# Optimization experiments

Hardware: AMD Instinct MI355X
Metric: run time of the kernel (lower is better)

The kernel has to match this reference:

```python
import jax, jax.numpy as jnp
import numpy as np

B, S, V, D = 8, 1024, 8192, 256
MAX_POS = 1024


def _positional_encoding(position, d_model):
    pos = np.arange(position)[:, None].astype(np.float32)
    i = np.arange(d_model)[None, :].astype(np.float32)
    angle_rads = pos / np.power(10000.0, 2.0 * np.floor(i / 2.0) / np.float32(d_model))
    angle_rads[:, 0::2] = np.sin(angle_rads[:, 0::2])
    angle_rads[:, 1::2] = np.cos(angle_rads[:, 1::2])
    return jnp.asarray(angle_rads[None, ...], dtype=jnp.float32)  # [1, position, d_model]


def setup_inputs() -> dict:
    key = jax.random.key(0)
    k1, k2 = jax.random.split(key)
    x = jax.random.randint(k1, (B, S, V), 0, 2, dtype=jnp.int32)  # multi-hot mask
    emb_table = jax.random.normal(k2, (V, D), dtype=jnp.float32) * 0.02
    pos_enc = _positional_encoding(MAX_POS, D)
    return {"x": x, "emb_table": emb_table, "pos_enc": pos_enc}


def reference(x, emb_table, pos_enc):
    # Multi-hot embedding-bag: sum_v x[b,s,v] * emb_table[v,:]  (dense O(V) reduction,
    # faithful to get_emb's full-vocab embed * mask + reduce_sum)
    seq_len = x.shape[1]
    d_model = emb_table.shape[1]
    xf = x.astype(jnp.float32)
    emb = jnp.einsum('bsv,vd->bsd', xf, emb_table)
    emb = emb * jnp.sqrt(jnp.float32(d_model))
    # positional encoding gated by whether the position has any active token
    any_tok = (jnp.sum(x, axis=-1) > 0).astype(jnp.float32)[..., None]  # [B,S,1]
    out = emb + pos_enc[:, :seq_len, :] * any_tok
    # dropout is identity in eval mode; num_layers = 0 -> no encoder layers
    return out
```

## Files before the change

kernel.cpp:

```cpp
#include <hip/hip_runtime.h>


#define M_TOT 8192
#define K_TOT 8192
#define D_DIM 256
#define KSPLIT 4
#define KCHUNK (K_TOT / KSPLIT)
#define BK 32

typedef short  short8  __attribute__((ext_vector_type(8)));
typedef float  floatx4 __attribute__((ext_vector_type(4)));
typedef int    intx4   __attribute__((ext_vector_type(4)));

#define WS_RS_OFF (4u * 1024u * 1024u)

__global__ __launch_bounds__(256) void zero_kernel(float* __restrict__ out, int* __restrict__ rs) {
    int b = blockIdx.x;
    if (b < 2048) {
        floatx4 z = {0.f, 0.f, 0.f, 0.f};
        *(floatx4*)(out + ((size_t)b * 256 + threadIdx.x) * 4) = z;
    } else {
        intx4 z = {0, 0, 0, 0};
        *(intx4*)(rs + ((size_t)(b - 2048) * 256 + threadIdx.x) * 4) = z;
    }
}

__global__ __launch_bounds__(256) void prep_kernel(const float* __restrict__ emb,
                                                   unsigned short* __restrict__ wsB) {
    __shared__ unsigned short tile[64][72];
    int v0 = blockIdx.x * 64, d0 = blockIdx.y * 64;
    int t = threadIdx.x;
    int r = t >> 2, c0 = (t & 3) * 16;
    const float* src = emb + (size_t)(v0 + r) * D_DIM + d0 + c0;
#pragma unroll
    for (int i = 0; i < 16; ++i) {
        unsigned int u = __float_as_uint(src[i] * 16.0f);
        u += 0x7fffu + ((u >> 16) & 1u);
        tile[c0 + i][r] = (unsigned short)(u >> 16);
    }
    __syncthreads();
    unsigned short* dst = wsB + (size_t)(d0 + r) * K_TOT + v0 + c0;
#pragma unroll
    for (int i = 0; i < 16; ++i) dst[i] = tile[r][c0 + i];
}

__global__ __launch_bounds__(256) void gemm_kernel(const int* __restrict__ x,
                                                   const unsigned short* __restrict__ wsB,
                                                   float* __restrict__ out,
                                                   int* __restrict__ rs) {
    __shared__ unsigned short Al[64][40];

    const int m0   = blockIdx.x * 64;
    const int kbeg = blockIdx.y * KCHUNK;
    const int t    = threadIdx.x;
    const int wave = t >> 6, lane = t & 63;
    const int quad = lane >> 4, rl = lane & 15;
    const int n0   = wave * 64;

    const int arow = t >> 2, akp = (t & 3) * 8;
    const int* aptr = x + (size_t)(m0 + arow) * K_TOT + kbeg + akp;

    floatx4 acc[4][4];
#pragma unroll
    for (int i = 0; i < 4; ++i)
#pragma unroll
        for (int j = 0; j < 4; ++j) acc[i][j] = (floatx4){0.f, 0.f, 0.f, 0.f};

    int rsum = 0;

    for (int kk = 0; kk < KCHUNK; kk += BK) {
        intx4 a0 = *(const intx4*)aptr;
        intx4 a1 = *(const intx4*)(aptr + 4);
        aptr += BK;

        short8 bf[4];
#pragma unroll
        for (int j = 0; j < 4; ++j) {
            const unsigned short* bp = wsB + (size_t)(n0 + j * 16 + rl) * K_TOT + kbeg + kk + quad * 8;
            bf[j] = *(const short8*)bp;
        }

        short8 av;
#pragma unroll
        for (int i = 0; i < 4; ++i) { av[i]     = a0[i] ? (short)0x3F80 : (short)0; rsum += a0[i]; }
#pragma unroll
        for (int i = 0; i < 4; ++i) { av[4 + i] = a1[i] ? (short)0x3F80 : (short)0; rsum += a1[i]; }

        __syncthreads();
        *(short8*)&Al[arow][akp] = av;
        __syncthreads();

        short8 af[4];
#pragma unroll
        for (int i = 0; i < 4; ++i)
            af[i] = *(const short8*)&Al[i * 16 + rl][quad * 8];

#pragma unroll
        for (int i = 0; i < 4; ++i)
#pragma unroll
            for (int j = 0; j < 4; ++j)
                acc[i][j] = __builtin_amdgcn_mfma_f32_16x16x32_bf16(af[i], bf[j], acc[i][j], 0, 0, 0);
    }

    rsum += __shfl_down(rsum, 1);
    rsum += __shfl_down(rsum, 2);
    if ((t & 3) == 0) atomicAdd(&rs[m0 + arow], rsum);

#pragma unroll
    for (int i = 0; i < 4; ++i) {
#pragma unroll
        for (int j = 0; j < 4; ++j) {
            int col = n0 + j * 16 + rl;
#pragma unroll
            for (int r = 0; r < 4; ++r) {
                int row = m0 + i * 16 + quad * 4 + r;
                unsafeAtomicAdd(&out[(size_t)row * D_DIM + col], acc[i][j][r]);
            }
        }
    }
}

__global__ __launch_bounds__(256) void epi_kernel(float* __restrict__ out,
                                                  const float* __restrict__ pos,
                                                  const int* __restrict__ rs) {
    int gid  = blockIdx.x * 256 + threadIdx.x;
    int base = gid * 4;
    int row  = base >> 8;
    int col  = base & 255;
    if (rs[row] > 0) {
        int s = row & 1023;
        floatx4 o = *(floatx4*)(out + base);
        floatx4 p = *(const floatx4*)(pos + (size_t)s * D_DIM + col);
        o += p;
        *(floatx4*)(out + base) = o;
    }
}

extern "C" void kernel_launch(void* const* d_in, const int* in_sizes, int n_in,
                              void* d_out, int out_size, void* d_ws, size_t ws_size,
                              hipStream_t stream) {
    const int*   x   = (const int*)d_in[0];
    const float* emb = (const float*)d_in[1];
    const float* pos = (const float*)d_in[2];
    float*       out = (float*)d_out;

    unsigned short* wsB = (unsigned short*)d_ws;
    int*            rs  = (int*)((char*)d_ws + WS_RS_OFF);

    zero_kernel<<<dim3(2056), dim3(256), 0, stream>>>(out, rs);
    prep_kernel<<<dim3(128, 4), dim3(256), 0, stream>>>(emb, wsB);
    gemm_kernel<<<dim3(128, KSPLIT), dim3(256), 0, stream>>>(x, wsB, out, rs);
    epi_kernel<<<dim3(2048), dim3(256), 0, stream>>>(out, pos, rs);
}
```

Baseline: 431.7 us.

## Pre-swizzle B into MFMA fragment layout, load A directly without LDS, split K 8-way

The prep kernel now writes the bf16 embedding table in an MFMA-fragment-ordered layout, so each lane fetches its B fragment with one contiguous 16-byte load. The GEMM drops the LDS staging and barriers for A: each wave reads the int mask straight from global memory and builds bf16 fragments by packing pairs of 0/1 values and multiplying by 0x3F80. K-split goes from 4 to 8 to launch more blocks, and the loop is unrolled by 2. The trade-off is that all four waves now read the same A rows redundantly from global or cache, and the larger split doubles the atomic adds into the output.

```diff
diff --git a/kernel.cpp b/kernel.cpp
--- a/kernel.cpp
+++ b/kernel.cpp
@@ -4,7 +4,7 @@
 #define M_TOT 8192
 #define K_TOT 8192
 #define D_DIM 256
-#define KSPLIT 4
+#define KSPLIT 8
 #define KCHUNK (K_TOT / KSPLIT)
 #define BK 32
 
@@ -12,7 +12,15 @@
 typedef float  floatx4 __attribute__((ext_vector_type(4)));
 typedef int    intx4   __attribute__((ext_vector_type(4)));
 
+union S8U { intx4 i; short8 s; };
+
 #define WS_RS_OFF (4u * 1024u * 1024u)
+
+__device__ __forceinline__ unsigned int bf16_rne(float f) {
+    unsigned int u = __float_as_uint(f);
+    u += 0x7fffu + ((u >> 16) & 1u);
+    return u >> 16;
+}
 
 __global__ __launch_bounds__(256) void zero_kernel(float* __restrict__ out, int* __restrict__ rs) {
     int b = blockIdx.x;
@@ -26,30 +34,28 @@
 }
 
 __global__ __launch_bounds__(256) void prep_kernel(const float* __restrict__ emb,
-                                                   unsigned short* __restrict__ wsB) {
-    __shared__ unsigned short tile[64][72];
-    int v0 = blockIdx.x * 64, d0 = blockIdx.y * 64;
-    int t = threadIdx.x;
-    int r = t >> 2, c0 = (t & 3) * 16;
-    const float* src = emb + (size_t)(v0 + r) * D_DIM + d0 + c0;
+                                                   unsigned short* __restrict__ wsBf) {
+    int gid = blockIdx.x * 256 + threadIdx.x;
+    int l  = gid & 63;
+    int kb = (gid >> 6) & 255;
+    int c  = gid >> 14;
+    int d  = c * 16 + (l & 15);
+    int v0 = kb * 32 + (l >> 4) * 8;
+    const float* src = emb + (size_t)v0 * D_DIM + d;
+    intx4 q;
 #pragma unroll
-    for (int i = 0; i < 16; ++i) {
-        unsigned int u = __float_as_uint(src[i] * 16.0f);
-        u += 0x7fffu + ((u >> 16) & 1u);
-        tile[c0 + i][r] = (unsigned short)(u >> 16);
+    for (int p = 0; p < 4; ++p) {
+        unsigned int u0 = bf16_rne(src[(size_t)(2 * p) * D_DIM] * 16.0f);
+        unsigned int u1 = bf16_rne(src[(size_t)(2 * p + 1) * D_DIM] * 16.0f);
+        q[p] = (int)(u0 | (u1 << 16));
     }
-    __syncthreads();
-    unsigned short* dst = wsB + (size_t)(d0 + r) * K_TOT + v0 + c0;
-#pragma unroll
-    for (int i = 0; i < 16; ++i) dst[i] = tile[r][c0 + i];
+    *(intx4*)(wsBf + (size_t)gid * 8) = q;
 }
 
 __global__ __launch_bounds__(256) void gemm_kernel(const int* __restrict__ x,
-                                                   const unsigned short* __restrict__ wsB,
+                                                   const unsigned short* __restrict__ wsBf,
                                                    float* __restrict__ out,
                                                    int* __restrict__ rs) {
-    __shared__ unsigned short Al[64][40];
-
     const int m0   = blockIdx.x * 64;
     const int kbeg = blockIdx.y * KCHUNK;
     const int t    = threadIdx.x;
@@ -57,43 +63,44 @@
     const int quad = lane >> 4, rl = lane & 15;
     const int n0   = wave * 64;
 
-    const int arow = t >> 2, akp = (t & 3) * 8;
-    const int* aptr = x + (size_t)(m0 + arow) * K_TOT + kbeg + akp;
-
     floatx4 acc[4][4];
 #pragma unroll
     for (int i = 0; i < 4; ++i)
 #pragma unroll
         for (int j = 0; j < 4; ++j) acc[i][j] = (floatx4){0.f, 0.f, 0.f, 0.f};
 
-    int rsum = 0;
+    int rp[4] = {0, 0, 0, 0};
 
+    const int* abase = x + (size_t)(m0 + rl) * K_TOT + kbeg + quad * 8;
+    const unsigned short* bbase = wsBf + ((size_t)(n0 >> 4) * 256) * 512 + (size_t)lane * 8;
+
+#pragma unroll 2
     for (int kk = 0; kk < KCHUNK; kk += BK) {
-        intx4 a0 = *(const intx4*)aptr;
-        intx4 a1 = *(const intx4*)(aptr + 4);
-        aptr += BK;
+        const int kb = (kbeg + kk) >> 5;
 
         short8 bf[4];
 #pragma unroll
-        for (int j = 0; j < 4; ++j) {
-            const unsigned short* bp = wsB + (size_t)(n0 + j * 16 + rl) * K_TOT + kbeg + kk + quad * 8;
-            bf[j] = *(const short8*)bp;
-        }
-
-        short8 av;
-#pragma unroll
-        for (int i = 0; i < 4; ++i) { av[i]     = a0[i] ? (short)0x3F80 : (short)0; rsum += a0[i]; }
-#pragma unroll
-        for (int i = 0; i < 4; ++i) { av[4 + i] = a1[i] ? (short)0x3F80 : (short)0; rsum += a1[i]; }
-
-        __syncthreads();
-        *(short8*)&Al[arow][akp] = av;
-        __syncthreads();
+        for (int j = 0; j < 4; ++j)
+            bf[j] = ((const S8U*)(bbase + ((size_t)j * 256 + kb) * 512))->s;
 
         short8 af[4];
 #pragma unroll
-        for (int i = 0; i < 4; ++i)
-            af[i] = *(const short8*)&Al[i * 16 + rl][quad * 8];
+        for (int i = 0; i < 4; ++i) {
+            const int* p = abase + (size_t)(i * 16) * K_TOT + kk;
+            intx4 a0 = *(const intx4*)p;
+            intx4 a1 = *(const intx4*)(p + 4);
+            int p0 = a0[0] | (a0[1] << 16);
+            int p1 = a0[2] | (a0[3] << 16);
+            int p2 = a1[0] | (a1[1] << 16);
+            int p3 = a1[2] | (a1[3] << 16);
+            if (wave == 0) rp[i] += p0 + p1 + p2 + p3;
+            S8U u;
+            u.i[0] = p0 * 0x3F80;
+            u.i[1] = p1 * 0x3F80;
+            u.i[2] = p2 * 0x3F80;
+            u.i[3] = p3 * 0x3F80;
+            af[i] = u.s;
+        }
 
 #pragma unroll
         for (int i = 0; i < 4; ++i)
@@ -102,9 +109,15 @@
                 acc[i][j] = __builtin_amdgcn_mfma_f32_16x16x32_bf16(af[i], bf[j], acc[i][j], 0, 0, 0);
     }
 
-    rsum += __shfl_down(rsum, 1);
-    rsum += __shfl_down(rsum, 2);
-    if ((t & 3) == 0) atomicAdd(&rs[m0 + arow], rsum);
+    if (wave == 0) {
+#pragma unroll
+        for (int i = 0; i < 4; ++i) {
+            int cnt = (rp[i] & 0xFFFF) + (rp[i] >> 16);
+            cnt += __shfl_xor(cnt, 16);
+            cnt += __shfl_xor(cnt, 32);
+            if (quad == 0) atomicAdd(&rs[m0 + i * 16 + rl], cnt);
+        }
+    }
 
 #pragma unroll
     for (int i = 0; i < 4; ++i) {
@@ -144,11 +157,11 @@
     const float* pos = (const float*)d_in[2];
     float*       out = (float*)d_out;
 
-    unsigned short* wsB = (unsigned short*)d_ws;
-    int*            rs  = (int*)((char*)d_ws + WS_RS_OFF);
+    unsigned short* wsBf = (unsigned short*)d_ws;
+    int*            rs   = (int*)((char*)d_ws + WS_RS_OFF);
 
     zero_kernel<<<dim3(2056), dim3(256), 0, stream>>>(out, rs);
-    prep_kernel<<<dim3(128, 4), dim3(256), 0, stream>>>(emb, wsB);
-    gemm_kernel<<<dim3(128, KSPLIT), dim3(256), 0, stream>>>(x, wsB, out, rs);
+    prep_kernel<<<dim3(1024), dim3(256), 0, stream>>>(emb, wsBf);
+    gemm_kernel<<<dim3(128, KSPLIT), dim3(256), 0, stream>>>(x, wsBf, out, rs);
     epi_kernel<<<dim3(2048), dim3(256), 0, stream>>>(out, pos, rs);
 }
```

After: 475.4 us. 10.1% more time.
